# Optimization experiments

Hardware: AMD Instinct MI355X
Metric: run time of the kernel (lower is better)

## Reference

```python
import jax, jax.numpy as jnp
import numpy as np
from jax import lax

UNIT = 0.11  # pairing threshold from sort_w(weight, 0.11)


def _greedy_pairs(wflat, unit=UNIT):
    """Faithful greedy pairing from sort_w: for each out-channel dd, scan flat
    indices a ascending; pair a with the first unoccupied b>a with
    |w[a]+w[b]|<=unit. Returns gather indices src and signs such that
    Weff[dd,i] = sign[dd,i] * Wflat[dd, src[dd,i]] reproduces vicsum_v2."""
    d, m = wflat.shape
    src = np.tile(np.arange(m, dtype=np.int32), (d, 1))
    sign = np.ones((d, m), dtype=np.float32)
    for dd in range(d):
        occ = np.zeros(m, dtype=bool)
        row = wflat[dd]
        for a in range(m - 1):
            if occ[a]:
                continue
            cand = np.nonzero((~occ[a + 1:]) & (np.abs(row[a] + row[a + 1:]) <= unit))[0]
            if cand.size:
                b = a + 1 + int(cand[0])
                occ[a] = occ[b] = True
                src[dd, b] = a     # out += (x[a]-x[b])*w[a]  =>  coeff at b is -w[a]
                sign[dd, b] = -1.0
    return src, sign


def _make_conv(rng, d, c, k):
    bound = 1.0 / np.sqrt(c * k * k)  # torch default uniform init scale
    w = rng.uniform(-bound, bound, size=(d, c, k, k)).astype(np.float32)
    b = rng.uniform(-bound, bound, size=(d,)).astype(np.float32)
    src, sign = _greedy_pairs(w.reshape(d, -1))
    return w, b, src, sign


def setup_inputs() -> dict:
    rng = np.random.default_rng(0)
    x = rng.standard_normal((16384, 1, 32, 32)).astype(np.float32)
    w1, b1, src1, sign1 = _make_conv(rng, 6, 1, 5)
    w2, b2, src2, sign2 = _make_conv(rng, 16, 6, 5)
    w3, b3, src3, sign3 = _make_conv(rng, 120, 16, 5)
    bf1 = 1.0 / np.sqrt(120.0)
    fc1_w = rng.uniform(-bf1, bf1, size=(84, 120)).astype(np.float32)
    fc1_b = rng.uniform(-bf1, bf1, size=(84,)).astype(np.float32)
    bf2 = 1.0 / np.sqrt(84.0)
    fc2_w = rng.uniform(-bf2, bf2, size=(10, 84)).astype(np.float32)
    fc2_b = rng.uniform(-bf2, bf2, size=(10,)).astype(np.float32)
    return {
        'x': jnp.asarray(x),
        'w1': jnp.asarray(w1), 'b1': jnp.asarray(b1), 'sign1': jnp.asarray(sign1),
        'w2': jnp.asarray(w2), 'b2': jnp.asarray(b2), 'sign2': jnp.asarray(sign2),
        'w3': jnp.asarray(w3), 'b3': jnp.asarray(b3), 'sign3': jnp.asarray(sign3),
        'fc1_w': jnp.asarray(fc1_w), 'fc1_b': jnp.asarray(fc1_b),
        'fc2_w': jnp.asarray(fc2_w), 'fc2_b': jnp.asarray(fc2_b),
        'src1': jnp.asarray(src1), 'src2': jnp.asarray(src2), 'src3': jnp.asarray(src3),
        'TRIGGERed': 1, 'count': 0,
    }


def _eff_weight(w, src, sign):
    d = w.shape[0]
    wflat = w.reshape(d, -1)
    weff = jnp.take_along_axis(wflat, src, axis=1) * sign
    return weff.reshape(w.shape)


def _conv(x, w, b):
    y = lax.conv_general_dilated(x, w, window_strides=(1, 1), padding='VALID',
                                 dimension_numbers=('NCHW', 'OIHW', 'NCHW'))
    return y + b[None, :, None, None]


def _avgpool2(x):
    n, c, h, w = x.shape
    return x.reshape(n, c, h // 2, 2, w // 2, 2).mean(axis=(3, 5))


def reference(x, w1, b1, sign1, w2, b2, sign2, w3, b3, sign3,
              fc1_w, fc1_b, fc2_w, fc2_b, src1, src2, src3, TRIGGERed, count):
    if TRIGGERed:
        h = _avgpool2(jax.nn.sigmoid(_conv(x, _eff_weight(w1, src1, sign1), b1)))
        h = _avgpool2(jax.nn.sigmoid(_conv(h, _eff_weight(w2, src2, sign2), b2)))
        h = jax.nn.sigmoid(_conv(h, _eff_weight(w3, src3, sign3), b3))
    else:
        h = _avgpool2(jax.nn.sigmoid(_conv(x, w1, b1)))
        h = _avgpool2(jax.nn.sigmoid(_conv(h, w2, b2)))
        h = jax.nn.sigmoid(_conv(h, w3, b3))
    h = h.reshape(h.shape[0], -1)                     # [N, 120]
    h = jax.nn.sigmoid(h @ fc1_w.T + fc1_b)           # [N, 84]
    return h @ fc2_w.T + fc2_b                        # [N, 10]
```

## Files before the change

### kernel.cpp

```cpp
#include <hip/hip_runtime.h>

#define THREADS 256

__device__ __forceinline__ float sigmoidf(float x) {
    return __builtin_amdgcn_rcpf(1.0f + __expf(-x));
}

#define E2OFF 168
#define E3OFF 2856
#define P1OFF 54056

__global__ void weff_prep(const float* __restrict__ w1, const float* __restrict__ sg1, const int* __restrict__ sr1,
                          const float* __restrict__ w2, const float* __restrict__ sg2, const int* __restrict__ sr2,
                          const float* __restrict__ w3, const float* __restrict__ sg3, const int* __restrict__ sr3,
                          const int* __restrict__ trig, float* __restrict__ ws) {
    int i = blockIdx.x * blockDim.x + threadIdx.x;
    const int t = trig[0];
    if (i < 168) {
        int c = i / 28, k = i % 28;
        float v = 0.f;
        if (k < 25) { int f = c * 25 + k; v = t ? sg1[f] * w1[c * 25 + sr1[f]] : w1[f]; }
        ws[i] = v;
    } else if (i < E3OFF) {
        int j = i - E2OFF;
        int oc = j / 168, r = j % 168, ic = r / 28, k = r % 28;
        float v = 0.f;
        if (k < 25) { int f = oc * 150 + ic * 25 + k; v = t ? sg2[f] * w2[oc * 150 + sr2[f]] : w2[f]; }
        ws[i] = v;
    } else if (i < P1OFF) {
        int idx = i - E3OFF;
        int j  = idx & 3;
        int l  = (idx >> 2) & 63;
        int kw = idx >> 8;
        int k  = kw % 50, wt = kw / 50;
        int c  = (wt << 5) | (l >> 1);
        int h  = l & 1;
        float v = 0.f;
        if (c < 120) {
            int e = c * 400 + h * 200 + k * 4 + j;
            v = t ? sg3[e] * w3[c * 400 + sr3[e]] : w3[e];
        }
        ws[i] = v;
    }
}

__global__ __launch_bounds__(THREADS, 4)
void k_conv1(const float* __restrict__ x, const float* __restrict__ ws,
             const float* __restrict__ b1, float* __restrict__ p1, int nimg) {
    __shared__ __align__(16) float lw[176];
    const int tid = threadIdx.x;
    if (tid < 168) lw[tid] = ws[tid];
    if (tid >= 168 && tid < 174) lw[tid] = b1[tid - 168];
    __syncthreads();

    int g = blockIdx.x * THREADS + tid;
    if (g >= nimg * 98) return;
    const int img = g / 98, rem = g % 98;
    const int r = rem / 7, t = rem % 7;

    const float* xb = x + (size_t)img * 1024 + (2 * r) * 32 + 4 * t;
    float pt[6][8];
    #pragma unroll
    for (int rr = 0; rr < 6; ++rr) {
        const float4 v0 = *reinterpret_cast<const float4*>(xb + rr * 32);
        const float4 v1 = *reinterpret_cast<const float4*>(xb + rr * 32 + 4);
        pt[rr][0] = v0.x; pt[rr][1] = v0.y; pt[rr][2] = v0.z; pt[rr][3] = v0.w;
        pt[rr][4] = v1.x; pt[rr][5] = v1.y; pt[rr][6] = v1.z; pt[rr][7] = v1.w;
    }

    #pragma unroll
    for (int c = 0; c < 6; ++c) {
        float z[2][4];
        #pragma unroll
        for (int p = 0; p < 2; ++p)
            #pragma unroll
            for (int w = 0; w < 4; ++w) z[p][w] = 0.f;

        #pragma unroll
        for (int k4 = 0; k4 < 6; ++k4) {
            const float4 w4 = *reinterpret_cast<const float4*>(&lw[c * 28 + 4 * k4]);
            #pragma unroll
            for (int j = 0; j < 4; ++j) {
                const int k = 4 * k4 + j;
                const int ky = k / 5, kx = k % 5;
                const float wv = (j == 0) ? w4.x : (j == 1) ? w4.y : (j == 2) ? w4.z : w4.w;
                #pragma unroll
                for (int p = 0; p < 2; ++p)
                    #pragma unroll
                    for (int dy = 0; dy < 2; ++dy)
                        #pragma unroll
                        for (int dx = 0; dx < 2; ++dx)
                            z[p][2 * dy + dx] += pt[dy + ky][2 * p + dx + kx] * wv;
            }
        }
        {
            const float wv = lw[c * 28 + 24];
            #pragma unroll
            for (int p = 0; p < 2; ++p)
                #pragma unroll
                for (int dy = 0; dy < 2; ++dy)
                    #pragma unroll
                    for (int dx = 0; dx < 2; ++dx)
                        z[p][2 * dy + dx] += pt[dy + 4][2 * p + dx + 4] * wv;
        }

        const float bb = lw[168 + c];
        const float s0 = sigmoidf(z[0][0] + bb) + sigmoidf(z[0][1] + bb) +
                         sigmoidf(z[0][2] + bb) + sigmoidf(z[0][3] + bb);
        const float s1 = sigmoidf(z[1][0] + bb) + sigmoidf(z[1][1] + bb) +
                         sigmoidf(z[1][2] + bb) + sigmoidf(z[1][3] + bb);
        *reinterpret_cast<float2*>(&p1[((size_t)img * 6 + c) * 196 + r * 14 + 2 * t]) =
            make_float2(0.25f * s0, 0.25f * s1);
    }
}

__global__ __launch_bounds__(THREADS, 3)
void k_conv2(const float* __restrict__ p1, const float* __restrict__ ws,
             const float* __restrict__ b2, float* __restrict__ p2, int nimg) {
    __shared__ __align__(16) float lw[2704];
    const int tid = threadIdx.x;
    for (int i = tid; i < 2688; i += THREADS) lw[i] = ws[E2OFF + i];
    if (tid < 16) lw[2688 + tid] = b2[tid];
    __syncthreads();

    const int npair = (nimg + 1) >> 1;
    int g = blockIdx.x * THREADS + tid;
    if (g >= npair * 25) return;
    const int pr = g / 25, pix = g % 25;
    const int imgA = 2 * pr;
    const int imgB = min(imgA + 1, nimg - 1);
    const int pi = pix / 5, pj = pix % 5;
    const float* pAb = p1 + (size_t)imgA * 1176 + (2 * pi) * 14 + 2 * pj;
    const float* pBb = p1 + (size_t)imgB * 1176 + (2 * pi) * 14 + 2 * pj;

    #pragma unroll 1
    for (int half = 0; half < 2; ++half) {
        float acc[8][4][2];
        #pragma unroll
        for (int oc = 0; oc < 8; ++oc)
            #pragma unroll
            for (int w = 0; w < 4; ++w) { acc[oc][w][0] = 0.f; acc[oc][w][1] = 0.f; }

        for (int ic = 0; ic < 6; ++ic) {
            float ptA[6][6], ptB[6][6];
            {
                const float* pa = pAb + ic * 196;
                const float* pb = pBb + ic * 196;
                #pragma unroll
                for (int r = 0; r < 6; ++r) {
                    #pragma unroll
                    for (int cc = 0; cc < 3; ++cc) {
                        float2 va = *reinterpret_cast<const float2*>(pa + r * 14 + 2 * cc);
                        float2 vb = *reinterpret_cast<const float2*>(pb + r * 14 + 2 * cc);
                        ptA[r][2 * cc] = va.x; ptA[r][2 * cc + 1] = va.y;
                        ptB[r][2 * cc] = vb.x; ptB[r][2 * cc + 1] = vb.y;
                    }
                }
            }
            const int wbase = half * 1344 + ic * 28;
            #pragma unroll
            for (int oc = 0; oc < 8; ++oc) {
                const int b = wbase + oc * 168;
                #pragma unroll
                for (int k4 = 0; k4 < 6; ++k4) {
                    const float4 w4 = *reinterpret_cast<const float4*>(&lw[b + 4 * k4]);
                    #pragma unroll
                    for (int j = 0; j < 4; ++j) {
                        const int k = 4 * k4 + j;
                        const int ky = k / 5, kx = k % 5;
                        const float wv = (j == 0) ? w4.x : (j == 1) ? w4.y : (j == 2) ? w4.z : w4.w;
                        acc[oc][0][0] += ptA[ky][kx] * wv;
                        acc[oc][1][0] += ptA[ky][kx + 1] * wv;
                        acc[oc][2][0] += ptA[ky + 1][kx] * wv;
                        acc[oc][3][0] += ptA[ky + 1][kx + 1] * wv;
                        acc[oc][0][1] += ptB[ky][kx] * wv;
                        acc[oc][1][1] += ptB[ky][kx + 1] * wv;
                        acc[oc][2][1] += ptB[ky + 1][kx] * wv;
                        acc[oc][3][1] += ptB[ky + 1][kx + 1] * wv;
                    }
                }
                const float wv = lw[b + 24];
                acc[oc][0][0] += ptA[4][4] * wv; acc[oc][1][0] += ptA[4][5] * wv;
                acc[oc][2][0] += ptA[5][4] * wv; acc[oc][3][0] += ptA[5][5] * wv;
                acc[oc][0][1] += ptB[4][4] * wv; acc[oc][1][1] += ptB[4][5] * wv;
                acc[oc][2][1] += ptB[5][4] * wv; acc[oc][3][1] += ptB[5][5] * wv;
            }
        }

        #pragma unroll
        for (int oc = 0; oc < 8; ++oc) {
            const int c = half * 8 + oc;
            const float bb = lw[2688 + c];
            const float sA = sigmoidf(acc[oc][0][0] + bb) + sigmoidf(acc[oc][1][0] + bb) +
                             sigmoidf(acc[oc][2][0] + bb) + sigmoidf(acc[oc][3][0] + bb);
            const float sB = sigmoidf(acc[oc][0][1] + bb) + sigmoidf(acc[oc][1][1] + bb) +
                             sigmoidf(acc[oc][2][1] + bb) + sigmoidf(acc[oc][3][1] + bb);
            p2[(size_t)imgA * 400 + c * 25 + pix] = 0.25f * sA;
            p2[(size_t)imgB * 400 + c * 25 + pix] = 0.25f * sB;
        }
    }
}

#define K3_IMG 8
__global__ __launch_bounds__(THREADS, 4)
void k_tail(const float* __restrict__ p2, const float* __restrict__ ws,
            const float* __restrict__ b3,
            const float* __restrict__ fc1w, const float* __restrict__ fc1b,
            const float* __restrict__ fc2w, const float* __restrict__ fc2b,
            float* __restrict__ out, int nimg) {
    __shared__ __align__(16) float sp2[K3_IMG][400];
    __shared__ __align__(16) float v3[K3_IMG][120];
    __shared__ __align__(16) float v4[K3_IMG][84];
    const int tid = threadIdx.x;
    const int img0 = blockIdx.x * K3_IMG;

    for (int i = tid; i < K3_IMG * 100; i += THREADS) {
        const int im = i / 100, off = i % 100;
        const int gi = min(img0 + im, nimg - 1);
        reinterpret_cast<float4*>(&sp2[im][0])[off] =
            reinterpret_cast<const float4*>(p2 + (size_t)gi * 400)[off];
    }
    __syncthreads();

    if (tid < 240) {
        const int h = tid & 1;
        const int wt = tid >> 6, l = tid & 63;
        const float4* wp = reinterpret_cast<const float4*>(ws + E3OFF);
        float4 a[K3_IMG];
        #pragma unroll
        for (int im = 0; im < K3_IMG; ++im) a[im] = make_float4(0.f, 0.f, 0.f, 0.f);
        #pragma unroll 5
        for (int k = 0; k < 50; ++k) {
            const float4 w4 = wp[(wt * 50 + k) * 64 + l];
            #pragma unroll
            for (int im = 0; im < K3_IMG; ++im) {
                const float4 u = *reinterpret_cast<const float4*>(&sp2[im][h * 200 + 4 * k]);
                a[im].x += u.x * w4.x; a[im].y += u.y * w4.y;
                a[im].z += u.z * w4.z; a[im].w += u.w * w4.w;
            }
        }
        const int c = tid >> 1;
        #pragma unroll
        for (int im = 0; im < K3_IMG; ++im) {
            float z = (a[im].x + a[im].y) + (a[im].z + a[im].w);
            z += __shfl_xor(z, 1, 64);
            if (h == 0) v3[im][c] = sigmoidf(z + b3[c]);
        }
    }
    __syncthreads();

    for (int it = tid; it < K3_IMG * 84; it += THREADS) {
        const int im = it / 84, j = it % 84;
        const float4* wp = reinterpret_cast<const float4*>(fc1w + j * 120);
        const float4* vp = reinterpret_cast<const float4*>(&v3[im][0]);
        float4 a = make_float4(0.f, 0.f, 0.f, 0.f);
        #pragma unroll 6
        for (int k = 0; k < 30; ++k) {
            const float4 w4 = wp[k];
            const float4 u = vp[k];
            a.x += u.x * w4.x; a.y += u.y * w4.y;
            a.z += u.z * w4.z; a.w += u.w * w4.w;
        }
        v4[im][j] = sigmoidf((a.x + a.y) + (a.z + a.w) + fc1b[j]);
    }
    __syncthreads();

    if (tid < K3_IMG * 10) {
        const int im = tid / 10, j = tid % 10;
        if (img0 + im < nimg) {
            const float4* wp = reinterpret_cast<const float4*>(fc2w + j * 84);
            const float4* vp = reinterpret_cast<const float4*>(&v4[im][0]);
            float4 a = make_float4(0.f, 0.f, 0.f, 0.f);
            #pragma unroll
            for (int k = 0; k < 21; ++k) {
                const float4 w4 = wp[k];
                const float4 u = vp[k];
                a.x += u.x * w4.x; a.y += u.y * w4.y;
                a.z += u.z * w4.z; a.w += u.w * w4.w;
            }
            out[(size_t)(img0 + im) * 10 + j] = (a.x + a.y) + (a.z + a.w) + fc2b[j];
        }
    }
}

__device__ __forceinline__ float wget_ig(const float* __restrict__ wp,
                                         const float* __restrict__ sg,
                                         const int* __restrict__ sr,
                                         int row, int m, int idx, bool tg) {
    int f = row * m + idx;
    return tg ? sg[f] * wp[row * m + sr[f]] : wp[f];
}

__global__ __launch_bounds__(THREADS, 4)
void lenet_fused(const float* __restrict__ x,
                 const float* __restrict__ w1e, const float* __restrict__ b1,
                 const float* __restrict__ w2e, const float* __restrict__ b2,
                 const float* __restrict__ w3e, const float* __restrict__ b3,
                 const float* __restrict__ fc1w, const float* __restrict__ fc1b,
                 const float* __restrict__ fc2w, const float* __restrict__ fc2b,
                 const float* __restrict__ sg1, const int* __restrict__ sr1,
                 const float* __restrict__ sg2, const int* __restrict__ sr2,
                 const float* __restrict__ sg3, const int* __restrict__ sr3,
                 const int* __restrict__ trig,
                 float* __restrict__ out, int nimg) {
    const int tid = threadIdx.x;
    const int img0 = blockIdx.x * 2;
    __shared__ __align__(16) float xs[2][1024];
    __shared__ __align__(16) float p1[2][6][196];
    __shared__ __align__(16) float p2[2][400];
    __shared__ __align__(16) float v3[2][120];
    __shared__ __align__(16) float v4[2][84];
    const bool tg = trig[0] != 0;

    #pragma unroll
    for (int im = 0; im < 2; ++im) {
        int gi = min(img0 + im, nimg - 1);
        reinterpret_cast<float4*>(&xs[im][0])[tid] =
            reinterpret_cast<const float4*>(x + (size_t)gi * 1024)[tid];
    }
    __syncthreads();

    for (int it = tid; it < 2 * 196; it += THREADS) {
        const int img = it / 196, pix = it % 196;
        const int pi = pix / 14, pj = pix % 14;
        const float* xb = &xs[img][(2 * pi) * 32 + 2 * pj];
        float pt[6][6];
        #pragma unroll
        for (int r = 0; r < 6; ++r)
            #pragma unroll
            for (int cc = 0; cc < 3; ++cc) {
                float2 v = *reinterpret_cast<const float2*>(&xb[r * 32 + cc * 2]);
                pt[r][cc * 2] = v.x; pt[r][cc * 2 + 1] = v.y;
            }
        #pragma unroll
        for (int c = 0; c < 6; ++c) {
            float z0 = 0.f, z1 = 0.f, z2 = 0.f, z3 = 0.f;
            #pragma unroll
            for (int ky = 0; ky < 5; ++ky)
                #pragma unroll
                for (int kx = 0; kx < 5; ++kx) {
                    const float wv = wget_ig(w1e, sg1, sr1, c, 25, ky * 5 + kx, tg);
                    z0 += pt[ky][kx] * wv;     z1 += pt[ky][kx + 1] * wv;
                    z2 += pt[ky + 1][kx] * wv; z3 += pt[ky + 1][kx + 1] * wv;
                }
            const float bb = b1[c];
            p1[img][c][pix] = 0.25f * (sigmoidf(z0 + bb) + sigmoidf(z1 + bb) +
                                       sigmoidf(z2 + bb) + sigmoidf(z3 + bb));
        }
    }
    __syncthreads();

    if (tid < 200) {
        const int img = tid / 100, rem = tid % 100;
        const int pix = rem >> 2, win = rem & 3;
        const int di = win >> 1, dj = win & 1;
        const int pi = pix / 5, pj = pix % 5;
        const int r0 = 2 * pi + di, c0 = 2 * pj + dj;
        float acc[16];
        #pragma unroll
        for (int c = 0; c < 16; ++c) acc[c] = 0.f;
        for (int ic = 0; ic < 6; ++ic) {
            float pt[5][5];
            #pragma unroll
            for (int ky = 0; ky < 5; ++ky)
                #pragma unroll
                for (int kx = 0; kx < 5; ++kx)
                    pt[ky][kx] = p1[img][ic][(r0 + ky) * 14 + (c0 + kx)];
            #pragma unroll
            for (int c = 0; c < 16; ++c) {
                float z = acc[c];
                #pragma unroll
                for (int ky = 0; ky < 5; ++ky)
                    #pragma unroll
                    for (int kx = 0; kx < 5; ++kx)
                        z += pt[ky][kx] * wget_ig(w2e, sg2, sr2, c, 150, ic * 25 + ky * 5 + kx, tg);
                acc[c] = z;
            }
        }
        #pragma unroll
        for (int c = 0; c < 16; ++c) {
            float z = sigmoidf(acc[c] + b2[c]);
            z += __shfl_xor(z, 1, 64);
            z += __shfl_xor(z, 2, 64);
            if (win == 0) p2[img][c * 25 + pix] = 0.25f * z;
        }
    }
    __syncthreads();

    if (tid < 240) {
        const int c = tid >> 1, h = tid & 1;
        float s0 = 0.f, s1 = 0.f;
        for (int k = 0; k < 200; ++k) {
            float wv = wget_ig(w3e, sg3, sr3, c, 400, h * 200 + k, tg);
            s0 += p2[0][h * 200 + k] * wv;
            s1 += p2[1][h * 200 + k] * wv;
        }
        s0 += __shfl_xor(s0, 1, 64);
        s1 += __shfl_xor(s1, 1, 64);
        if (h == 0) {
            const float bb = b3[c];
            v3[0][c] = sigmoidf(s0 + bb);
            v3[1][c] = sigmoidf(s1 + bb);
        }
    }
    __syncthreads();

    if (tid < 168) {
        const int img = tid / 84, j = tid % 84;
        float a = 0.f;
        for (int k = 0; k < 120; ++k) a += v3[img][k] * fc1w[j * 120 + k];
        v4[img][j] = sigmoidf(a + fc1b[j]);
    }
    __syncthreads();

    if (tid < 20) {
        const int img = tid / 10, j = tid % 10;
        if (img0 + img < nimg) {
            float a = 0.f;
            for (int k = 0; k < 84; ++k) a += v4[img][k] * fc2w[j * 84 + k];
            out[(size_t)(img0 + img) * 10 + j] = a + fc2b[j];
        }
    }
}

extern "C" void kernel_launch(void* const* d_in, const int* in_sizes, int n_in,
                              void* d_out, int out_size, void* d_ws, size_t ws_size,
                              hipStream_t stream) {
    const float* x    = (const float*)d_in[0];
    const float* w1   = (const float*)d_in[1];
    const float* b1   = (const float*)d_in[2];
    const float* sg1  = (const float*)d_in[3];
    const float* w2   = (const float*)d_in[4];
    const float* b2   = (const float*)d_in[5];
    const float* sg2  = (const float*)d_in[6];
    const float* w3   = (const float*)d_in[7];
    const float* b3   = (const float*)d_in[8];
    const float* sg3  = (const float*)d_in[9];
    const float* fc1w = (const float*)d_in[10];
    const float* fc1b = (const float*)d_in[11];
    const float* fc2w = (const float*)d_in[12];
    const float* fc2b = (const float*)d_in[13];
    const int*   sr1  = (const int*)d_in[14];
    const int*   sr2  = (const int*)d_in[15];
    const int*   sr3  = (const int*)d_in[16];
    const int*   trig = (const int*)d_in[17];

    const int nimg = in_sizes[0] / 1024;
    float* out = (float*)d_out;

    const size_t p1off = P1OFF;
    const size_t p2off = p1off + (size_t)nimg * 1176;
    const size_t need_bytes = (p2off + (size_t)nimg * 400) * sizeof(float);

    if (ws_size >= need_bytes) {
        float* ws = (float*)d_ws;
        weff_prep<<<(P1OFF + 255) / 256, 256, 0, stream>>>(
            w1, sg1, sr1, w2, sg2, sr2, w3, sg3, sr3, trig, ws);
        k_conv1<<<(nimg * 98 + THREADS - 1) / THREADS, THREADS, 0, stream>>>(
            x, ws, b1, ws + p1off, nimg);
        const int npair = (nimg + 1) / 2;
        k_conv2<<<(npair * 25 + THREADS - 1) / THREADS, THREADS, 0, stream>>>(
            ws + p1off, ws, b2, ws + p2off, nimg);
        k_tail<<<(nimg + K3_IMG - 1) / K3_IMG, THREADS, 0, stream>>>(
            ws + p2off, ws, b3, fc1w, fc1b, fc2w, fc2b, out, nimg);
    } else {
        lenet_fused<<<(nimg + 1) / 2, THREADS, 0, stream>>>(
            x, w1, b1, w2, b2, w3, b3,
            fc1w, fc1b, fc2w, fc2b, sg1, sr1, sg2, sr2, sg3, sr3, trig, out, nimg);
    }
}
```

Measured before the change: 259.8 us.

## Drop two-image register blocking and LDS weight staging in conv2

Each conv2 thread now computes one image instead of two, which halves the accumulator and patch registers and doubles the thread count. The shared-memory weight copy and its barrier are removed, so weights and bias are read directly from global memory and served by the scalar or L1 cache. The cost is that each weight load is amortised over half as many FMAs, and there are more global weight reads in exchange for less register pressure and no LDS setup.

```diff
diff --git a/kernel.cpp b/kernel.cpp
--- a/kernel.cpp
+++ b/kernel.cpp
@@ -117,86 +117,63 @@
 __global__ __launch_bounds__(THREADS, 3)
 void k_conv2(const float* __restrict__ p1, const float* __restrict__ ws,
              const float* __restrict__ b2, float* __restrict__ p2, int nimg) {
-    __shared__ __align__(16) float lw[2704];
-    const int tid = threadIdx.x;
-    for (int i = tid; i < 2688; i += THREADS) lw[i] = ws[E2OFF + i];
-    if (tid < 16) lw[2688 + tid] = b2[tid];
-    __syncthreads();
-
-    const int npair = (nimg + 1) >> 1;
-    int g = blockIdx.x * THREADS + tid;
-    if (g >= npair * 25) return;
-    const int pr = g / 25, pix = g % 25;
-    const int imgA = 2 * pr;
-    const int imgB = min(imgA + 1, nimg - 1);
+    int g = blockIdx.x * THREADS + threadIdx.x;
+    if (g >= nimg * 25) return;
+    const int img = g / 25, pix = g % 25;
     const int pi = pix / 5, pj = pix % 5;
-    const float* pAb = p1 + (size_t)imgA * 1176 + (2 * pi) * 14 + 2 * pj;
-    const float* pBb = p1 + (size_t)imgB * 1176 + (2 * pi) * 14 + 2 * pj;
+    const float* pimg = p1 + (size_t)img * 1176 + (2 * pi) * 14 + 2 * pj;
+    const float* wq = ws + E2OFF;
 
     #pragma unroll 1
     for (int half = 0; half < 2; ++half) {
-        float acc[8][4][2];
+        float acc[8][4];
         #pragma unroll
         for (int oc = 0; oc < 8; ++oc)
             #pragma unroll
-            for (int w = 0; w < 4; ++w) { acc[oc][w][0] = 0.f; acc[oc][w][1] = 0.f; }
+            for (int w = 0; w < 4; ++w) acc[oc][w] = 0.f;
 
         for (int ic = 0; ic < 6; ++ic) {
-            float ptA[6][6], ptB[6][6];
-            {
-                const float* pa = pAb + ic * 196;
-                const float* pb = pBb + ic * 196;
-                #pragma unroll
-                for (int r = 0; r < 6; ++r) {
-                    #pragma unroll
-                    for (int cc = 0; cc < 3; ++cc) {
-                        float2 va = *reinterpret_cast<const float2*>(pa + r * 14 + 2 * cc);
-                        float2 vb = *reinterpret_cast<const float2*>(pb + r * 14 + 2 * cc);
-                        ptA[r][2 * cc] = va.x; ptA[r][2 * cc + 1] = va.y;
-                        ptB[r][2 * cc] = vb.x; ptB[r][2 * cc + 1] = vb.y;
-                    }
+            float pt[6][6];
+            const float* pb = pimg + ic * 196;
+            #pragma unroll
+            for (int r = 0; r < 6; ++r) {
+                #pragma unroll
+                for (int cc = 0; cc < 3; ++cc) {
+                    float2 v = *reinterpret_cast<const float2*>(pb + r * 14 + 2 * cc);
+                    pt[r][2 * cc] = v.x; pt[r][2 * cc + 1] = v.y;
                 }
             }
             const int wbase = half * 1344 + ic * 28;
             #pragma unroll
             for (int oc = 0; oc < 8; ++oc) {
-                const int b = wbase + oc * 168;
+                const float* wr = wq + wbase + oc * 168;
                 #pragma unroll
                 for (int k4 = 0; k4 < 6; ++k4) {
-                    const float4 w4 = *reinterpret_cast<const float4*>(&lw[b + 4 * k4]);
+                    const float4 w4 = *reinterpret_cast<const float4*>(wr + 4 * k4);
                     #pragma unroll
                     for (int j = 0; j < 4; ++j) {
                         const int k = 4 * k4 + j;
                         const int ky = k / 5, kx = k % 5;
                         const float wv = (j == 0) ? w4.x : (j == 1) ? w4.y : (j == 2) ? w4.z : w4.w;
-                        acc[oc][0][0] += ptA[ky][kx] * wv;
-                        acc[oc][1][0] += ptA[ky][kx + 1] * wv;
-                        acc[oc][2][0] += ptA[ky + 1][kx] * wv;
-                        acc[oc][3][0] += ptA[ky + 1][kx + 1] * wv;
-                        acc[oc][0][1] += ptB[ky][kx] * wv;
-                        acc[oc][1][1] += ptB[ky][kx + 1] * wv;
-                        acc[oc][2][1] += ptB[ky + 1][kx] * wv;
-                        acc[oc][3][1] += ptB[ky + 1][kx + 1] * wv;
+                        acc[oc][0] += pt[ky][kx] * wv;
+                        acc[oc][1] += pt[ky][kx + 1] * wv;
+                        acc[oc][2] += pt[ky + 1][kx] * wv;
+                        acc[oc][3] += pt[ky + 1][kx + 1] * wv;
                     }
                 }
-                const float wv = lw[b + 24];
-                acc[oc][0][0] += ptA[4][4] * wv; acc[oc][1][0] += ptA[4][5] * wv;
-                acc[oc][2][0] += ptA[5][4] * wv; acc[oc][3][0] += ptA[5][5] * wv;
-                acc[oc][0][1] += ptB[4][4] * wv; acc[oc][1][1] += ptB[4][5] * wv;
-                acc[oc][2][1] += ptB[5][4] * wv; acc[oc][3][1] += ptB[5][5] * wv;
+                const float wv = wr[24];
+                acc[oc][0] += pt[4][4] * wv; acc[oc][1] += pt[4][5] * wv;
+                acc[oc][2] += pt[5][4] * wv; acc[oc][3] += pt[5][5] * wv;
             }
         }
 
         #pragma unroll
         for (int oc = 0; oc < 8; ++oc) {
             const int c = half * 8 + oc;
-            const float bb = lw[2688 + c];
-            const float sA = sigmoidf(acc[oc][0][0] + bb) + sigmoidf(acc[oc][1][0] + bb) +
-                             sigmoidf(acc[oc][2][0] + bb) + sigmoidf(acc[oc][3][0] + bb);
-            const float sB = sigmoidf(acc[oc][0][1] + bb) + sigmoidf(acc[oc][1][1] + bb) +
-                             sigmoidf(acc[oc][2][1] + bb) + sigmoidf(acc[oc][3][1] + bb);
-            p2[(size_t)imgA * 400 + c * 25 + pix] = 0.25f * sA;
-            p2[(size_t)imgB * 400 + c * 25 + pix] = 0.25f * sB;
+            const float bb = b2[c];
+            const float s = sigmoidf(acc[oc][0] + bb) + sigmoidf(acc[oc][1] + bb) +
+                            sigmoidf(acc[oc][2] + bb) + sigmoidf(acc[oc][3] + bb);
+            p2[(size_t)img * 400 + c * 25 + pix] = 0.25f * s;
         }
     }
 }
@@ -458,8 +435,7 @@
             w1, sg1, sr1, w2, sg2, sr2, w3, sg3, sr3, trig, ws);
         k_conv1<<<(nimg * 98 + THREADS - 1) / THREADS, THREADS, 0, stream>>>(
             x, ws, b1, ws + p1off, nimg);
-        const int npair = (nimg + 1) / 2;
-        k_conv2<<<(npair * 25 + THREADS - 1) / THREADS, THREADS, 0, stream>>>(
+        k_conv2<<<(nimg * 25 + THREADS - 1) / THREADS, THREADS, 0, stream>>>(
             ws + p1off, ws, b2, ws + p2off, nimg);
         k_tail<<<(nimg + K3_IMG - 1) / K3_IMG, THREADS, 0, stream>>>(
             ws + p2off, ws, b3, fc1w, fc1b, fc2w, fc2b, out, nimg);
```

New measurement: 232.7 us. 10.4% less time.
